# Kernel tuning notes

Hardware: AMD Instinct MI355X
Metric: run time of the kernel (lower is better)

## Reference

```python
import jax, jax.numpy as jnp
import numpy as np

N, E, IN_C, OUT_C, HEADS = 50000, 800000, 256, 256, 4
C = OUT_C // HEADS  # per-head channels = 64
BN_EPS = 1e-5


def setup_inputs() -> dict:
    key = jax.random.key(0)
    ks = jax.random.split(key, 16)
    inp = {
        'x': jax.random.normal(ks[0], (N, IN_C), dtype=jnp.float32),
        'edge_index': jax.random.randint(ks[1], (2, E), 0, N, dtype=jnp.int64),
        'edge_attr': jax.random.uniform(ks[2], (E, 1), dtype=jnp.float32),
        'spatial_coords': jax.random.normal(ks[3], (N, 2), dtype=jnp.float32),
        # GATConv params
        'W_gat': jax.random.normal(ks[4], (IN_C, HEADS * C), dtype=jnp.float32) * 0.05,
        'att_src': jax.random.normal(ks[5], (HEADS, C), dtype=jnp.float32) * 0.05,
        'att_dst': jax.random.normal(ks[6], (HEADS, C), dtype=jnp.float32) * 0.05,
        'bias_gat': jnp.zeros((HEADS * C,), dtype=jnp.float32),
        # spatial_attention MLP (computed but unused by the original forward)
        'w1': jax.random.normal(ks[7], (1, 64), dtype=jnp.float32) * 0.05,
        'b1': jnp.zeros((64,), dtype=jnp.float32),
        'w2': jax.random.normal(ks[8], (64, HEADS), dtype=jnp.float32) * 0.05,
        'b2': jnp.zeros((HEADS,), dtype=jnp.float32),
        # feature_transform: Linear + BatchNorm1d (eval stats) + ReLU (+Dropout=identity)
        'w_ft': jax.random.normal(ks[9], (IN_C, OUT_C), dtype=jnp.float32) * 0.05,
        'b_ft': jnp.zeros((OUT_C,), dtype=jnp.float32),
        'bn_gamma': jnp.ones((OUT_C,), dtype=jnp.float32),
        'bn_beta': jnp.zeros((OUT_C,), dtype=jnp.float32),
        'bn_mean': jax.random.normal(ks[10], (OUT_C,), dtype=jnp.float32) * 0.01,
        'bn_var': jax.random.uniform(ks[11], (OUT_C,), dtype=jnp.float32, minval=0.5, maxval=1.5),
    }
    return inp


def _forward(x, edge_index, edge_attr, W_gat, att_src, att_dst, bias_gat,
             w1, b1, w2, b2, w_ft, b_ft, bn_gamma, bn_beta, bn_mean, bn_var):
    n = x.shape[0]
    # add self-loops (PyG GATConv default)
    loop = jnp.arange(n, dtype=edge_index.dtype)
    src = jnp.concatenate([edge_index[0], loop])
    dst = jnp.concatenate([edge_index[1], loop])

    # linear transform: [N, heads, C]
    h = (x @ W_gat).reshape(n, HEADS, C)
    a_src = jnp.einsum('nhc,hc->nh', h, att_src)  # [N, H]
    a_dst = jnp.einsum('nhc,hc->nh', h, att_dst)  # [N, H]

    # per-edge attention logits, LeakyReLU(0.2)
    alpha = jax.nn.leaky_relu(a_src[src] + a_dst[dst], negative_slope=0.2)  # [Etot, H]
    # segment softmax over incoming edges of each destination node
    amax = jax.ops.segment_max(alpha, dst, num_segments=n)
    alpha = jnp.exp(alpha - amax[dst])
    denom = jax.ops.segment_sum(alpha, dst, num_segments=n)
    alpha = alpha / (denom[dst] + 1e-16)

    # weighted message aggregation
    msg = h[src] * alpha[:, :, None]                        # [Etot, H, C]
    agg = jax.ops.segment_sum(msg, dst, num_segments=n)     # [N, H, C]
    gat_out = agg.reshape(n, HEADS * C) + bias_gat

    # spatial attention weights (computed but UNUSED, matching original)
    spatial_weights = jax.nn.sigmoid(jax.nn.relu(edge_attr @ w1 + b1) @ w2 + b2)
    del spatial_weights

    # feature_transform (BatchNorm in eval mode, Dropout identity)
    y = x @ w_ft + b_ft
    y = (y - bn_mean) * jax.lax.rsqrt(bn_var + BN_EPS) * bn_gamma + bn_beta
    transformed = jax.nn.relu(y)

    return gat_out + transformed


def reference(x, edge_index, edge_attr, spatial_coords, W_gat, att_src, att_dst,
              bias_gat, w1, b1, w2, b2, w_ft, b_ft, bn_gamma, bn_beta, bn_mean, bn_var):
    # spatial_coords is accepted but unused by the original module's forward
    return _forward(x, edge_index, edge_attr, W_gat, att_src, att_dst, bias_gat,
                    w1, b1, w2, b2, w_ft, b_ft, bn_gamma, bn_beta, bn_mean, bn_var)
```

## Files before the change

### kernel.cpp

```cpp
#include <hip/hip_runtime.h>
#include <math.h>

typedef __attribute__((ext_vector_type(4))) float  f32x4;
typedef __attribute__((ext_vector_type(8))) short  short8;
typedef __attribute__((ext_vector_type(4))) unsigned short usx4;
typedef __attribute__((ext_vector_type(8))) unsigned short usx8;

__device__ __forceinline__ float bf2f(unsigned short u) {
    union { unsigned int i; float f; } c; c.i = ((unsigned int)u) << 16; return c.f;
}
__device__ __forceinline__ unsigned short f2bf(float f) {
    union { float f; unsigned int i; } c; c.f = f;
    unsigned int x = c.i;
    unsigned int r = (x + 0x7FFFu + ((x >> 16) & 1u)) >> 16;
    return (unsigned short)r;
}

__global__ __launch_bounds__(256) void k_convert_w(const float* __restrict__ Wg,
                                                   const float* __restrict__ Wf,
                                                   unsigned short* __restrict__ wbt) {
    int idx = blockIdx.x * blockDim.x + threadIdx.x;
    if (idx >= 512 * 256) return;
    int c = idx >> 8;
    int k = idx & 255;
    float v = (c < 256) ? Wg[k * 256 + c] : Wf[k * 256 + (c - 256)];
    wbt[idx] = f2bf(v);
}

#define BM 128
#define BN 128
#define BK 32
__global__ __launch_bounds__(256) void k_gemm(
    const float* __restrict__ x,
    const unsigned short* __restrict__ wbt,
    unsigned short* __restrict__ hb,
    unsigned short* __restrict__ tb,
    float* __restrict__ out,
    const float* __restrict__ b_ft, const float* __restrict__ bn_g,
    const float* __restrict__ bn_b, const float* __restrict__ bn_m,
    const float* __restrict__ bn_v, int M) {
    __shared__ unsigned short As[BM][BK + 8];
    __shared__ unsigned short Bs[BN][BK + 8];
    const int t = threadIdx.x;
    const int w = t >> 6, lane = t & 63;
    const int wr = w >> 1, wc = w & 1;
    const int bm0 = blockIdx.x * BM;
    const int bn0 = blockIdx.y * BN;
    const int kg = lane >> 4;
    const int lm = lane & 15;

    f32x4 acc[4][4] = {};

    for (int k0 = 0; k0 < 256; k0 += BK) {
        f32x4 a0[2], a1[2];
        usx8 bv[2];
#pragma unroll
        for (int s = 0; s < 2; s++) {
            int seg = t + s * 256;
            int row = seg >> 2;
            int off = (seg & 3) * 8;
            int grow = bm0 + row; if (grow >= M) grow = M - 1;
            const float* ap = x + (long)grow * 256 + k0 + off;
            a0[s] = *(const f32x4*)ap;
            a1[s] = *(const f32x4*)(ap + 4);
            bv[s] = *(const usx8*)(wbt + (long)(bn0 + row) * 256 + k0 + off);
        }
        __syncthreads();
#pragma unroll
        for (int s = 0; s < 2; s++) {
            int seg = t + s * 256;
            int row = seg >> 2;
            int off = (seg & 3) * 8;
            usx8 av;
            av[0] = f2bf(a0[s][0]); av[1] = f2bf(a0[s][1]);
            av[2] = f2bf(a0[s][2]); av[3] = f2bf(a0[s][3]);
            av[4] = f2bf(a1[s][0]); av[5] = f2bf(a1[s][1]);
            av[6] = f2bf(a1[s][2]); av[7] = f2bf(a1[s][3]);
            *(usx8*)&As[row][off] = av;
            *(usx8*)&Bs[row][off] = bv[s];
        }
        __syncthreads();
        short8 afr[4], bfr[4];
#pragma unroll
        for (int mi = 0; mi < 4; mi++)
            afr[mi] = *(const short8*)&As[wr * 64 + mi * 16 + lm][kg * 8];
#pragma unroll
        for (int nj = 0; nj < 4; nj++)
            bfr[nj] = *(const short8*)&Bs[wc * 64 + nj * 16 + lm][kg * 8];
#pragma unroll
        for (int mi = 0; mi < 4; mi++)
#pragma unroll
            for (int nj = 0; nj < 4; nj++)
                acc[mi][nj] = __builtin_amdgcn_mfma_f32_16x16x32_bf16(
                    afr[mi], bfr[nj], acc[mi][nj], 0, 0, 0);
        __syncthreads();
    }

    const bool isH = (bn0 < 256);
#pragma unroll
    for (int mi = 0; mi < 4; mi++) {
#pragma unroll
        for (int nj = 0; nj < 4; nj++) {
            int col = bn0 + wc * 64 + nj * 16 + lm;
            f32x4 a = acc[mi][nj];
            int rowbase = bm0 + wr * 64 + mi * 16 + kg * 4;
            if (isH) {
#pragma unroll
                for (int r = 0; r < 4; r++) {
                    int row = rowbase + r;
                    if (row < M) hb[(long)row * 256 + col] = f2bf(a[r]);
                }
            } else {
                int c2 = col - 256;
                float bft = b_ft[c2], mu = bn_m[c2];
                float iv = rsqrtf(bn_v[c2] + 1e-5f);
                float g = bn_g[c2], bt = bn_b[c2];
#pragma unroll
                for (int r = 0; r < 4; r++) {
                    int row = rowbase + r;
                    if (row < M) {
                        float v = (a[r] + bft - mu) * iv * g + bt;
                        v = v > 0.f ? v : 0.f;
                        if (tb) tb[(long)row * 256 + c2] = f2bf(v);
                        else    out[(long)row * 256 + c2] = v;
                    }
                }
            }
        }
    }
}

__global__ __launch_bounds__(256) void k_attn(const unsigned short* __restrict__ hb,
                                              const float* __restrict__ att_s,
                                              const float* __restrict__ att_d,
                                              float* __restrict__ a_src,
                                              float* __restrict__ a_dst, int N) {
    int gid = blockIdx.x * 256 + threadIdx.x;
    int node = gid >> 6;
    int lane = threadIdx.x & 63;
    if (node >= N) return;
    usx4 hv = ((const usx4*)(hb + (long)node * 256))[lane];
    int head = lane >> 4;
    int cb = (lane & 15) * 4;
    float s1 = 0.f, s2 = 0.f;
#pragma unroll
    for (int j = 0; j < 4; j++) {
        float h = bf2f(hv[j]);
        s1 += h * att_s[head * 64 + cb + j];
        s2 += h * att_d[head * 64 + cb + j];
    }
#pragma unroll
    for (int o = 1; o < 16; o <<= 1) {
        s1 += __shfl_xor(s1, o);
        s2 += __shfl_xor(s2, o);
    }
    if ((lane & 15) == 0) {
        a_src[node * 4 + head] = s1;
        a_dst[node * 4 + head] = s2;
    }
}

__global__ void k_zero2(int* a, int* b, int n) {
    int i = blockIdx.x * blockDim.x + threadIdx.x;
    if (i < n) { a[i] = 0; b[i] = 0; }
}
__global__ void k_count(const int* __restrict__ ei, int* __restrict__ deg,
                        int E, int N) {
    int i = blockIdx.x * blockDim.x + threadIdx.x;
    if (i >= E + N) return;
    int d = (i < E) ? ei[E + i] : (i - E);
    atomicAdd(&deg[d], 1);
}
__global__ __launch_bounds__(256) void k_scan1(const int* __restrict__ deg,
                                               int* __restrict__ offs,
                                               int* __restrict__ bsum, int n) {
    __shared__ int tmp[256];
    int b = blockIdx.x, t = threadIdx.x;
    int base = b * 1024;
    int v[4];
#pragma unroll
    for (int j = 0; j < 4; j++) {
        int i = base + t * 4 + j;
        v[j] = (i < n) ? deg[i] : 0;
    }
    int local = v[0] + v[1] + v[2] + v[3];
    tmp[t] = local;
    __syncthreads();
    for (int off = 1; off < 256; off <<= 1) {
        int xv = (t >= off) ? tmp[t - off] : 0;
        __syncthreads();
        tmp[t] += xv;
        __syncthreads();
    }
    int run = tmp[t] - local;
    if (t == 255) bsum[b] = tmp[255];
#pragma unroll
    for (int j = 0; j < 4; j++) {
        int i = base + t * 4 + j;
        if (i < n) offs[i] = run;
        run += v[j];
    }
}
__global__ void k_scan2(int* bsum, int nb) {
    if (threadIdx.x == 0 && blockIdx.x == 0) {
        int acc = 0;
        for (int i = 0; i < nb; i++) { int x = bsum[i]; bsum[i] = acc; acc += x; }
    }
}
__global__ void k_scan3(int* offs, const int* bsum, int n) {
    int i = blockIdx.x * blockDim.x + threadIdx.x;
    if (i < n) offs[i] += bsum[i >> 10];
}
__global__ void k_scatter(const int* __restrict__ ei, const int* __restrict__ offs,
                          int* __restrict__ cursor, int* __restrict__ srcs, int E, int N) {
    int i = blockIdx.x * blockDim.x + threadIdx.x;
    if (i >= E + N) return;
    int d, s;
    if (i < E) { d = ei[E + i]; s = ei[i]; }
    else       { d = i - E;     s = i - E; }
    int pos = atomicAdd(&cursor[d], 1);
    srcs[offs[d] + pos] = s;
}

__global__ __launch_bounds__(256) void k_agg(
    const int* __restrict__ offs, const int* __restrict__ srcs,
    const unsigned short* __restrict__ hb,
    const float* __restrict__ a_src, const float* __restrict__ a_dst,
    const float* __restrict__ bias_gat, const unsigned short* __restrict__ tb,
    float* __restrict__ out, int N, int E) {
    const int n = blockIdx.x;
    const int t = threadIdx.x;
    const int p = t >> 6;
    const int l = t & 63;
    const int head = l >> 4;
    int beg = offs[n];
    int end = (n + 1 < N) ? offs[n + 1] : (E + N);

    __shared__ int   s_src[64];
    __shared__ float s_w[64][4];
    __shared__ float s_acc[4][64][4];
    __shared__ float s_den[4][4];

    const float ad = a_dst[(long)n * 4 + p];
    f32x4 acc = {};
    float den = 0.f;

    for (int base = beg; base < end; base += 64) {
        int len = min(64, end - base);
        {
            int j = l;
            int hh = p;
            float w = 0.f;
            int src = 0;
            if (j < len) {
                src = srcs[base + j];
                float lv = a_src[(long)src * 4 + hh] + ad;
                lv = fmaxf(lv, 0.2f * lv);
                w = __expf(lv);
            }
            s_w[j][hh] = w;
            if (hh == 0) s_src[j] = src;
        }
        __syncthreads();
        int lenp = (len + 3) & ~3;
        for (int i = 0; i < lenp; i += 4) {
            int slot = i + p;
            float w = s_w[slot][head];
            int src = s_src[slot];
            uint2 hv = ((const uint2*)(hb + ((long)src << 8)))[l];
            den += w;
            acc[0] = fmaf(w, __uint_as_float(hv.x << 16), acc[0]);
            acc[1] = fmaf(w, __uint_as_float(hv.x & 0xFFFF0000u), acc[1]);
            acc[2] = fmaf(w, __uint_as_float(hv.y << 16), acc[2]);
            acc[3] = fmaf(w, __uint_as_float(hv.y & 0xFFFF0000u), acc[3]);
        }
        __syncthreads();
    }

    *(f32x4*)&s_acc[p][l][0] = acc;
    if ((l & 15) == 0) s_den[p][l >> 4] = den;
    __syncthreads();
    if (t < 64) {
        int lc = t;
        int hh = lc >> 4;
        f32x4 a0 = *(const f32x4*)&s_acc[0][lc][0];
        f32x4 a1 = *(const f32x4*)&s_acc[1][lc][0];
        f32x4 a2 = *(const f32x4*)&s_acc[2][lc][0];
        f32x4 a3 = *(const f32x4*)&s_acc[3][lc][0];
        f32x4 asum = a0 + a1 + a2 + a3;
        float dtot = s_den[0][hh] + s_den[1][hh] + s_den[2][hh] + s_den[3][hh];
        float inv = 1.f / (dtot + 1e-16f);
        float4 bv = ((const float4*)bias_gat)[lc];
        float4 trf;
        long rowoff = (long)n * 256 + lc * 4;
        if (tb) {
            uint2 tv = ((const uint2*)(tb + (long)n * 256))[lc];
            trf.x = __uint_as_float(tv.x << 16);
            trf.y = __uint_as_float(tv.x & 0xFFFF0000u);
            trf.z = __uint_as_float(tv.y << 16);
            trf.w = __uint_as_float(tv.y & 0xFFFF0000u);
        } else {
            trf = *(const float4*)(out + rowoff);
        }
        float4 r;
        r.x = asum[0] * inv + bv.x + trf.x;
        r.y = asum[1] * inv + bv.y + trf.y;
        r.z = asum[2] * inv + bv.z + trf.z;
        r.w = asum[3] * inv + bv.w + trf.w;
        *(float4*)(out + rowoff) = r;
    }
}

extern "C" void kernel_launch(void* const* d_in, const int* in_sizes, int n_in,
                              void* d_out, int out_size, void* d_ws, size_t ws_size,
                              hipStream_t stream) {
    const float* x        = (const float*)d_in[0];
    const int*   ei       = (const int*)d_in[1];
    const float* W_gat    = (const float*)d_in[4];
    const float* att_src  = (const float*)d_in[5];
    const float* att_dst  = (const float*)d_in[6];
    const float* bias_gat = (const float*)d_in[7];
    const float* w_ft     = (const float*)d_in[12];
    const float* b_ft     = (const float*)d_in[13];
    const float* bn_g     = (const float*)d_in[14];
    const float* bn_b     = (const float*)d_in[15];
    const float* bn_m     = (const float*)d_in[16];
    const float* bn_v     = (const float*)d_in[17];
    float* out = (float*)d_out;

    const int N = in_sizes[0] / 256;
    const int E = in_sizes[1] / 2;
    const int ETOT = E + N;

    char* p = (char*)d_ws;
    char* pend = p + ws_size;
    auto alloc = [&](size_t bytes) {
        void* r = (void*)p;
        p += (bytes + 255) & ~(size_t)255;
        return r;
    };
    unsigned short* wbt  = (unsigned short*)alloc((size_t)512 * 256 * 2);
    unsigned short* hb   = (unsigned short*)alloc((size_t)N * 256 * 2);
    float* a_src = (float*)alloc((size_t)N * 4 * 4);
    float* a_dst = (float*)alloc((size_t)N * 4 * 4);
    int* deg    = (int*)alloc((size_t)N * 4);
    int* cursor = (int*)alloc((size_t)N * 4);
    int* offs   = (int*)alloc((size_t)(N + 1) * 4);
    int* bsum   = (int*)alloc((size_t)256 * 4);
    int* srcs   = (int*)alloc((size_t)ETOT * 4);
    unsigned short* tb = (unsigned short*)alloc((size_t)N * 256 * 2);
    if (p > pend) tb = nullptr;

    k_convert_w<<<(512 * 256 + 255) / 256, 256, 0, stream>>>(W_gat, w_ft, wbt);

    dim3 gg((N + BM - 1) / BM, 4);
    k_gemm<<<gg, 256, 0, stream>>>(x, wbt, hb, tb, out, b_ft, bn_g, bn_b, bn_m, bn_v, N);

    k_attn<<<(N + 3) / 4, 256, 0, stream>>>(hb, att_src, att_dst, a_src, a_dst, N);

    k_zero2<<<(N + 255) / 256, 256, 0, stream>>>(deg, cursor, N);
    k_count<<<(ETOT + 255) / 256, 256, 0, stream>>>(ei, deg, E, N);
    int nb = (N + 1023) / 1024;
    k_scan1<<<nb, 256, 0, stream>>>(deg, offs, bsum, N);
    k_scan2<<<1, 64, 0, stream>>>(bsum, nb);
    k_scan3<<<(N + 255) / 256, 256, 0, stream>>>(offs, bsum, N);
    k_scatter<<<(ETOT + 255) / 256, 256, 0, stream>>>(ei, offs, cursor, srcs, E, N);

    k_agg<<<N, 256, 0, stream>>>(offs, srcs, hb, a_src, a_dst, bias_gat, tb, out, N, E);
}
```

Measured before the change: 274.8 us.

## Aggregate each destination node with one wavefront instead of a whole block

The aggregation kernel now gives each destination node a single 64-lane wavefront, four nodes per block, instead of a 256-thread block per node. Source indices are broadcast with shuffles, and each lane computes the attention weight for its own head inline. This removes shared memory, the __syncthreads barriers and the cross-wave reduction, and it fixes the lane waste that came from padding each node's edges to groups of four. The cost is less memory-level parallelism per node (one gather stream instead of four) and a redundant a_src load and exp in every lane. The zeroing kernel is also replaced by one hipMemsetAsync, which relies on deg and cursor being laid out contiguously in the workspace with 256-byte alignment.

```diff
diff --git a/kernel.cpp b/kernel.cpp
--- a/kernel.cpp
+++ b/kernel.cpp
@@ -160,10 +160,6 @@
     }
 }
 
-__global__ void k_zero2(int* a, int* b, int n) {
-    int i = blockIdx.x * blockDim.x + threadIdx.x;
-    if (i < n) { a[i] = 0; b[i] = 0; }
-}
 __global__ void k_count(const int* __restrict__ ei, int* __restrict__ deg,
                         int E, int N) {
     int i = blockIdx.x * blockDim.x + threadIdx.x;
@@ -228,87 +224,54 @@
     const float* __restrict__ a_src, const float* __restrict__ a_dst,
     const float* __restrict__ bias_gat, const unsigned short* __restrict__ tb,
     float* __restrict__ out, int N, int E) {
-    const int n = blockIdx.x;
-    const int t = threadIdx.x;
-    const int p = t >> 6;
-    const int l = t & 63;
+    const int n = (blockIdx.x * 256 + threadIdx.x) >> 6;
+    const int l = threadIdx.x & 63;
+    if (n >= N) return;
     const int head = l >> 4;
-    int beg = offs[n];
-    int end = (n + 1 < N) ? offs[n + 1] : (E + N);
-
-    __shared__ int   s_src[64];
-    __shared__ float s_w[64][4];
-    __shared__ float s_acc[4][64][4];
-    __shared__ float s_den[4][4];
-
-    const float ad = a_dst[(long)n * 4 + p];
+    const int beg = offs[n];
+    const int end = (n + 1 < N) ? offs[n + 1] : (E + N);
+
+    const float ad = a_dst[(long)n * 4 + head];
     f32x4 acc = {};
     float den = 0.f;
 
     for (int base = beg; base < end; base += 64) {
-        int len = min(64, end - base);
-        {
-            int j = l;
-            int hh = p;
-            float w = 0.f;
-            int src = 0;
-            if (j < len) {
-                src = srcs[base + j];
-                float lv = a_src[(long)src * 4 + hh] + ad;
-                lv = fmaxf(lv, 0.2f * lv);
-                w = __expf(lv);
-            }
-            s_w[j][hh] = w;
-            if (hh == 0) s_src[j] = src;
+        const int len = min(64, end - base);
+        int sv = (base + l < end) ? srcs[base + l] : 0;
+        for (int i = 0; i < len; ++i) {
+            int src = __shfl(sv, i);
+            float as = a_src[(long)src * 4 + head];
+            float lv = as + ad;
+            lv = fmaxf(lv, 0.2f * lv);
+            float wgt = __expf(lv);
+            uint2 hv = ((const uint2*)(hb + ((long)src << 8)))[l];
+            den += wgt;
+            acc[0] = fmaf(wgt, __uint_as_float(hv.x << 16), acc[0]);
+            acc[1] = fmaf(wgt, __uint_as_float(hv.x & 0xFFFF0000u), acc[1]);
+            acc[2] = fmaf(wgt, __uint_as_float(hv.y << 16), acc[2]);
+            acc[3] = fmaf(wgt, __uint_as_float(hv.y & 0xFFFF0000u), acc[3]);
         }
-        __syncthreads();
-        int lenp = (len + 3) & ~3;
-        for (int i = 0; i < lenp; i += 4) {
-            int slot = i + p;
-            float w = s_w[slot][head];
-            int src = s_src[slot];
-            uint2 hv = ((const uint2*)(hb + ((long)src << 8)))[l];
-            den += w;
-            acc[0] = fmaf(w, __uint_as_float(hv.x << 16), acc[0]);
-            acc[1] = fmaf(w, __uint_as_float(hv.x & 0xFFFF0000u), acc[1]);
-            acc[2] = fmaf(w, __uint_as_float(hv.y << 16), acc[2]);
-            acc[3] = fmaf(w, __uint_as_float(hv.y & 0xFFFF0000u), acc[3]);
-        }
-        __syncthreads();
-    }
-
-    *(f32x4*)&s_acc[p][l][0] = acc;
-    if ((l & 15) == 0) s_den[p][l >> 4] = den;
-    __syncthreads();
-    if (t < 64) {
-        int lc = t;
-        int hh = lc >> 4;
-        f32x4 a0 = *(const f32x4*)&s_acc[0][lc][0];
-        f32x4 a1 = *(const f32x4*)&s_acc[1][lc][0];
-        f32x4 a2 = *(const f32x4*)&s_acc[2][lc][0];
-        f32x4 a3 = *(const f32x4*)&s_acc[3][lc][0];
-        f32x4 asum = a0 + a1 + a2 + a3;
-        float dtot = s_den[0][hh] + s_den[1][hh] + s_den[2][hh] + s_den[3][hh];
-        float inv = 1.f / (dtot + 1e-16f);
-        float4 bv = ((const float4*)bias_gat)[lc];
-        float4 trf;
-        long rowoff = (long)n * 256 + lc * 4;
-        if (tb) {
-            uint2 tv = ((const uint2*)(tb + (long)n * 256))[lc];
-            trf.x = __uint_as_float(tv.x << 16);
-            trf.y = __uint_as_float(tv.x & 0xFFFF0000u);
-            trf.z = __uint_as_float(tv.y << 16);
-            trf.w = __uint_as_float(tv.y & 0xFFFF0000u);
-        } else {
-            trf = *(const float4*)(out + rowoff);
-        }
-        float4 r;
-        r.x = asum[0] * inv + bv.x + trf.x;
-        r.y = asum[1] * inv + bv.y + trf.y;
-        r.z = asum[2] * inv + bv.z + trf.z;
-        r.w = asum[3] * inv + bv.w + trf.w;
-        *(float4*)(out + rowoff) = r;
-    }
+    }
+
+    const float inv = 1.f / (den + 1e-16f);
+    const float4 bv = ((const float4*)bias_gat)[l];
+    float4 trf;
+    const long rowoff = ((long)n << 8) + l * 4;
+    if (tb) {
+        uint2 tv = ((const uint2*)(tb + ((long)n << 8)))[l];
+        trf.x = __uint_as_float(tv.x << 16);
+        trf.y = __uint_as_float(tv.x & 0xFFFF0000u);
+        trf.z = __uint_as_float(tv.y << 16);
+        trf.w = __uint_as_float(tv.y & 0xFFFF0000u);
+    } else {
+        trf = *(const float4*)(out + rowoff);
+    }
+    float4 r;
+    r.x = acc[0] * inv + bv.x + trf.x;
+    r.y = acc[1] * inv + bv.y + trf.y;
+    r.z = acc[2] * inv + bv.z + trf.z;
+    r.w = acc[3] * inv + bv.w + trf.w;
+    *(float4*)(out + rowoff) = r;
 }
 
 extern "C" void kernel_launch(void* const* d_in, const int* in_sizes, int n_in,
@@ -358,7 +321,7 @@
 
     k_attn<<<(N + 3) / 4, 256, 0, stream>>>(hb, att_src, att_dst, a_src, a_dst, N);
 
-    k_zero2<<<(N + 255) / 256, 256, 0, stream>>>(deg, cursor, N);
+    hipMemsetAsync(deg, 0, ((size_t)N * 4 + 255 & ~(size_t)255) + (size_t)N * 4, stream);
     k_count<<<(ETOT + 255) / 256, 256, 0, stream>>>(ei, deg, E, N);
     int nb = (N + 1023) / 1024;
     k_scan1<<<nb, 256, 0, stream>>>(deg, offs, bsum, N);
@@ -366,5 +329,6 @@
     k_scan3<<<(N + 255) / 256, 256, 0, stream>>>(offs, bsum, N);
     k_scatter<<<(ETOT + 255) / 256, 256, 0, stream>>>(ei, offs, cursor, srcs, E, N);
 
-    k_agg<<<N, 256, 0, stream>>>(offs, srcs, hb, a_src, a_dst, bias_gat, tb, out, N, E);
-}
+    k_agg<<<(N * 64 + 255) / 256, 256, 0, stream>>>(offs, srcs, hb, a_src, a_dst,
+                                                    bias_gat, tb, out, N, E);
+}
```

After: 260.6 us. 5.2% less time.
